# Kernel tuning notes

Hardware: AMD Instinct MI355X
Metric: run time of the kernel (lower is better)

The kernel has to match this reference:

```python
import jax, jax.numpy as jnp
import numpy as np

N_NODES = 50000
N_EDGES = 800000
D_IN, D_HID, D_OUT = 128, 96, 32


def _lin_params(key, d_in, d_out):
    k1, k2 = jax.random.split(key)
    bound = 1.0 / np.sqrt(d_in)
    W = jax.random.uniform(k1, (d_in, d_out), jnp.float32, -bound, bound)
    b = jax.random.uniform(k2, (d_out,), jnp.float32, -bound, bound)
    return W, b


def setup_inputs() -> dict:
    key = jax.random.key(0)
    ks = jax.random.split(key, 11)
    x = jax.random.normal(ks[0], (N_NODES, D_IN), jnp.float32)
    edge_index = jax.random.randint(ks[1], (2, N_EDGES), 0, N_NODES, jnp.int64)
    Wq1, bq1 = _lin_params(ks[2], D_IN, D_HID)
    Wk1, bk1 = _lin_params(ks[3], D_IN, D_HID)
    Wv1, bv1 = _lin_params(ks[4], D_IN, D_HID)
    Ws1, bs1 = _lin_params(ks[5], D_IN, D_HID)
    Wq2, bq2 = _lin_params(ks[6], D_HID, D_HID)
    Wk2, bk2 = _lin_params(ks[7], D_HID, D_HID)
    Wv2, bv2 = _lin_params(ks[8], D_HID, D_HID)
    Ws2, bs2 = _lin_params(ks[9], D_HID, D_HID)
    Wd, bd = _lin_params(ks[10], D_HID, D_OUT)
    return dict(x=x, edge_index=edge_index,
                Wq1=Wq1, bq1=bq1, Wk1=Wk1, bk1=bk1, Wv1=Wv1, bv1=bv1, Ws1=Ws1, bs1=bs1,
                Wq2=Wq2, bq2=bq2, Wk2=Wk2, bk2=bk2, Wv2=Wv2, bv2=bv2, Ws2=Ws2, bs2=bs2,
                Wd=Wd, bd=bd)


def transformer_conv(x, src, dst, Wq, bq, Wk, bk, Wv, bv, Ws, bs):
    # PyG TransformerConv, heads=1, concat=True, root_weight=True, edge_dim=None
    q = x @ Wq + bq  # [N, d]
    k = x @ Wk + bk
    v = x @ Wv + bv
    d = q.shape[-1]
    scale = 1.0 / np.sqrt(d).astype(np.float32)
    alpha = jnp.sum(q[dst] * k[src], axis=-1) * scale  # [E]
    # segment softmax over destination nodes
    m = jax.ops.segment_max(alpha, dst, num_segments=N_NODES)  # [N]
    e = jnp.exp(alpha - m[dst])
    s = jax.ops.segment_sum(e, dst, num_segments=N_NODES)
    w = e / (s[dst] + 1e-16)
    out = jax.ops.segment_sum(w[:, None] * v[src], dst, num_segments=N_NODES)  # [N, d]
    return out + x @ Ws + bs  # root/skip connection


def reference(x, edge_index,
              Wq1, bq1, Wk1, bk1, Wv1, bv1, Ws1, bs1,
              Wq2, bq2, Wk2, bk2, Wv2, bv2, Ws2, bs2,
              Wd, bd):
    src, dst = edge_index[0], edge_index[1]
    h = transformer_conv(x, src, dst, Wq1, bq1, Wk1, bk1, Wv1, bv1, Ws1, bs1)
    h = jax.nn.relu(h)
    h = transformer_conv(h, src, dst, Wq2, bq2, Wk2, bk2, Wv2, bv2, Ws2, bs2)
    return h @ Wd + bd
```

## Files before the change

kernel.cpp:

```cpp
#include <hip/hip_runtime.h>
#include <hip/hip_bf16.h>
#include <math.h>

#define NN_C 50000
#define NE_C 800000
#define NBKT 196
#define E_PER_BLK 4096
#define S1_BLOCKS 196
#define S2_CAP 8192

typedef short bf16x8 __attribute__((ext_vector_type(8)));
typedef float f32x4 __attribute__((ext_vector_type(4)));

__device__ inline float blo(unsigned int u) { return __uint_as_float(u << 16); }
__device__ inline float bhi(unsigned int u) { return __uint_as_float(u & 0xffff0000u); }

__device__ inline unsigned short bf16rne(float f) {
    union { __hip_bfloat16 h; unsigned short u; } c;
    c.h = __float2bfloat16(f);
    return c.u;
}
__device__ inline unsigned int pk2(float a, float b) {
    return (unsigned int)bf16rne(a) | ((unsigned int)bf16rne(b) << 16);
}

__device__ inline int block_incl_scan(int v, int lane, int wid, int* ws)
{
    int x = v;
    #pragma unroll
    for (int off = 1; off < 64; off <<= 1) {
        int t = __shfl_up(x, off);
        if (lane >= off) x += t;
    }
    if (lane == 63) ws[wid] = x;
    __syncthreads();
    int woff = 0;
    #pragma unroll
    for (int w = 0; w < 4; ++w)
        if (w < wid) woff += ws[w];
    return woff + x;
}

template<bool AF32>
__global__ __launch_bounds__(256) void gemm_mfma(
    const void* __restrict__ Ap, const unsigned short* __restrict__ Wt,
    const float* __restrict__ bias,
    unsigned short* __restrict__ aggb, unsigned short* __restrict__ qsb,
    int M)
{
    __shared__ char lds[65536];
    char* sA = lds;
    char* sB = lds + 32768;
    const int tid = threadIdx.x;
    const int r0 = blockIdx.x * 128;
    const int c0 = blockIdx.y * 128;
    const char* Wb = (const char*)Wt + (size_t)c0 * 256;

    if (AF32) {
        const char* Asrc = (const char*)Ap;
        #pragma unroll
        for (int sct = 0; sct < 8; ++sct) {
            int o = (sct * 256 + tid) * 16;
            int r = o >> 8;
            int gr = r0 + r; if (gr > M - 1) gr = M - 1;
            const char* p = Asrc + (size_t)gr * 512 + (o & 255) * 2;
            float4 a = *reinterpret_cast<const float4*>(p);
            float4 b = *reinterpret_cast<const float4*>(p + 16);
            uint4 val;
            val.x = pk2(a.x, a.y); val.y = pk2(a.z, a.w);
            val.z = pk2(b.x, b.y); val.w = pk2(b.z, b.w);
            *reinterpret_cast<uint4*>(sA + (o ^ ((r & 7) << 4))) = val;
        }
    } else {
        const char* Asrc = (const char*)Ap;
        #pragma unroll
        for (int sct = 0; sct < 8; ++sct) {
            int o = (sct * 256 + tid) * 16;
            int r = o >> 8;
            int gr = r0 + r; if (gr > M - 1) gr = M - 1;
            uint4 val = *reinterpret_cast<const uint4*>(Asrc + (size_t)gr * 256 + (o & 255));
            *reinterpret_cast<uint4*>(sA + (o ^ ((r & 7) << 4))) = val;
        }
    }
    #pragma unroll
    for (int sct = 0; sct < 8; ++sct) {
        int o = (sct * 256 + tid) * 16;
        int r = o >> 8;
        uint4 val = *reinterpret_cast<const uint4*>(Wb + o);
        *reinterpret_cast<uint4*>(sB + (o ^ ((r & 7) << 4))) = val;
    }
    __syncthreads();

    const int lane = tid & 63, wid = tid >> 6;
    const int wm = wid >> 1, wn = wid & 1;
    const int qw = lane >> 4, c16 = lane & 15;

    f32x4 acc[4][4];
    #pragma unroll
    for (int a = 0; a < 4; ++a)
        #pragma unroll
        for (int b = 0; b < 4; ++b) acc[a][b] = (f32x4){0.f, 0.f, 0.f, 0.f};

    int aoff[4], boff[4];
    #pragma unroll
    for (int fm = 0; fm < 4; ++fm) {
        int r = wm * 64 + fm * 16 + c16;
        aoff[fm] = r * 256 + ((qw * 16) ^ ((r & 7) << 4));
    }
    #pragma unroll
    for (int fn = 0; fn < 4; ++fn) {
        int r = wn * 64 + fn * 16 + c16;
        boff[fn] = r * 256 + ((qw * 16) ^ ((r & 7) << 4));
    }

    #pragma unroll
    for (int ks = 0; ks < 4; ++ks) {
        const int kx = ks * 64;
        bf16x8 af[4], bfr[4];
        #pragma unroll
        for (int fm = 0; fm < 4; ++fm)
            af[fm] = *reinterpret_cast<const bf16x8*>(sA + (aoff[fm] ^ kx));
        #pragma unroll
        for (int fn = 0; fn < 4; ++fn)
            bfr[fn] = *reinterpret_cast<const bf16x8*>(sB + (boff[fn] ^ kx));
        #pragma unroll
        for (int fm = 0; fm < 4; ++fm)
            #pragma unroll
            for (int fn = 0; fn < 4; ++fn)
                acc[fm][fn] = __builtin_amdgcn_mfma_f32_16x16x32_bf16(
                    af[fm], bfr[fn], acc[fm][fn], 0, 0, 0);
    }

    #pragma unroll
    for (int fn = 0; fn < 4; ++fn) {
        int colbase = c0 + wn * 64 + fn * 16;
        int g = colbase / 96;
        unsigned short* obuf; int elem0;
        if (g == 0)      { obuf = qsb;  elem0 = colbase; }
        else if (g == 3) { obuf = qsb;  elem0 = colbase - 192; }
        else             { obuf = aggb; elem0 = colbase - 96; }
        float bcol = bias[colbase + c16];
        #pragma unroll
        for (int fm = 0; fm < 4; ++fm) {
            #pragma unroll
            for (int j = 0; j < 4; ++j) {
                int rg = r0 + wm * 64 + fm * 16 + qw * 4 + j;
                float o = acc[fm][fn][j] + bcol;
                float o2 = __shfl_xor(o, 1);
                if (!(lane & 1) && rg < M) {
                    *reinterpret_cast<unsigned int*>(
                        (char*)obuf + (size_t)rg * 384 + (size_t)(elem0 + c16) * 2) = pk2(o, o2);
                }
            }
        }
    }
}

__global__ __launch_bounds__(256) void setup_kernel(
    const float* __restrict__ w0a, const float* __restrict__ w1a,
    const float* __restrict__ w2a, const float* __restrict__ w3a,
    const float* __restrict__ b0a, const float* __restrict__ b1a,
    const float* __restrict__ b2a, const float* __restrict__ b3a,
    const float* __restrict__ w0b, const float* __restrict__ w1b,
    const float* __restrict__ w2b, const float* __restrict__ w3b,
    const float* __restrict__ b0b, const float* __restrict__ b1b,
    const float* __restrict__ b2b, const float* __restrict__ b3b,
    const int* __restrict__ dst,
    unsigned short* __restrict__ WtA, float* __restrict__ b4a,
    unsigned short* __restrict__ WtB, float* __restrict__ b4b,
    int* __restrict__ bucketCnt)
{
    __shared__ int hist[NBKT];
    const int tid = threadIdx.x;
    const int blk = blockIdx.x;
    if (blk < 384) {
        const bool L2w = blk >= 192;
        int idx = (L2w ? blk - 192 : blk) * 256 + tid;
        int n = idx >> 7, k = idx & 127;
        int g = n / 96, c = n - g * 96;
        const float* w; const float* bb;
        if (!L2w) {
            w = (g == 0) ? w0a : (g == 1) ? w1a : (g == 2) ? w2a : w3a;
            bb = (g == 0) ? b0a : (g == 1) ? b1a : (g == 2) ? b2a : b3a;
            WtA[idx] = bf16rne((k < 128) ? w[(size_t)k * 96 + c] : 0.f);
            if (k == 0) b4a[n] = bb[c];
        } else {
            w = (g == 0) ? w0b : (g == 1) ? w1b : (g == 2) ? w2b : w3b;
            bb = (g == 0) ? b0b : (g == 1) ? b1b : (g == 2) ? b2b : b3b;
            WtB[idx] = bf16rne((k < 96) ? w[(size_t)k * 96 + c] : 0.f);
            if (k == 0) b4b[n] = bb[c];
        }
    } else {
        const int hb = blk - 384;
        for (int t = tid; t < NBKT; t += 256) hist[t] = 0;
        __syncthreads();
        const int e0 = hb * E_PER_BLK;
        const int ne = min(E_PER_BLK, NE_C - e0);
        for (int j = tid; j < ne; j += 256)
            atomicAdd(&hist[((unsigned)dst[e0 + j]) >> 8], 1);
        __syncthreads();
        for (int t = tid; t < NBKT; t += 256)
            if (hist[t]) atomicAdd(&bucketCnt[t], hist[t]);
    }
}

__global__ __launch_bounds__(256) void scanb_kernel(
    const int* __restrict__ bucketCnt, int* __restrict__ bucketBase,
    int* __restrict__ gCur)
{
    __shared__ int ws[4];
    const int tid = threadIdx.x;
    int v = (tid < NBKT) ? bucketCnt[tid] : 0;
    int incl = block_incl_scan(v, tid & 63, tid >> 6, ws);
    int excl = incl - v;
    if (tid < NBKT) { bucketBase[tid] = excl; gCur[tid] = excl; }
    if (tid == NBKT - 1) bucketBase[NBKT] = incl;
}

__global__ __launch_bounds__(256) void stage1_kernel(
    const int* __restrict__ src, const int* __restrict__ dst,
    int* __restrict__ gCur, unsigned int* __restrict__ bktArr)
{
    __shared__ int hist[NBKT], loff[NBKT], lcur[NBKT], gbase[NBKT];
    __shared__ unsigned int bufRaw[E_PER_BLK];
    __shared__ unsigned int buf[E_PER_BLK];
    __shared__ int ws[4];
    const int tid = threadIdx.x;
    const int e0 = blockIdx.x * E_PER_BLK;
    const int ne = min(E_PER_BLK, NE_C - e0);

    for (int t = tid; t < NBKT; t += 256) hist[t] = 0;
    __syncthreads();
    for (int j = tid; j < ne; j += 256) {
        int d = dst[e0 + j], s = src[e0 + j];
        unsigned int pk = ((unsigned)d << 16) | (unsigned)s;
        bufRaw[j] = pk;
        atomicAdd(&hist[(unsigned)d >> 8], 1);
    }
    __syncthreads();
    {
        int v = (tid < NBKT) ? hist[tid] : 0;
        int incl = block_incl_scan(v, tid & 63, tid >> 6, ws);
        if (tid < NBKT) { loff[tid] = incl - v; lcur[tid] = incl - v; }
    }
    __syncthreads();
    for (int j = tid; j < ne; j += 256) {
        unsigned int pk = bufRaw[j];
        int p = atomicAdd(&lcur[pk >> 24], 1);
        buf[p] = pk;
    }
    __syncthreads();
    if (tid < NBKT && hist[tid] > 0) gbase[tid] = atomicAdd(&gCur[tid], hist[tid]);
    __syncthreads();
    for (int j = tid; j < ne; j += 256) {
        unsigned int pk = buf[j];
        int b = pk >> 24;
        bktArr[gbase[b] + (j - loff[b])] = pk;
    }
}

__global__ __launch_bounds__(256) void stage2_kernel(
    const unsigned int* __restrict__ bktArr, const int* __restrict__ bucketBase,
    int* __restrict__ csr, int* __restrict__ row)
{
    __shared__ int ncnt[256], noff[256], ncur[256];
    __shared__ int outb[S2_CAP];
    __shared__ int ws[4];
    const int tid = threadIdx.x;
    const int b = blockIdx.x;
    const int base = bucketBase[b];
    const int cnt = bucketBase[b + 1] - base;

    ncnt[tid] = 0;
    __syncthreads();
    for (int j = tid; j < cnt; j += 256)
        atomicAdd(&ncnt[(bktArr[base + j] >> 16) & 255], 1);
    __syncthreads();
    {
        int v = ncnt[tid];
        int incl = block_incl_scan(v, tid & 63, tid >> 6, ws);
        noff[tid] = incl - v; ncur[tid] = incl - v;
    }
    __syncthreads();
    for (int j = tid; j < cnt; j += 256) {
        unsigned int pk = bktArr[base + j];
        int p = atomicAdd(&ncur[(pk >> 16) & 255], 1);
        if (p < S2_CAP) outb[p] = (int)(pk & 0xFFFFu);
    }
    __syncthreads();
    for (int j = tid; j < cnt && j < S2_CAP; j += 256) csr[base + j] = outb[j];
    const int node0 = b * 256;
    if (node0 + tid < NN_C) row[node0 + tid] = base + noff[tid];
    if (b == 0 && tid == 0) row[NN_C] = NE_C;
}

template<int MODE>
__global__ __launch_bounds__(256) void aggregate_kernel(
    const unsigned short* __restrict__ aggb, const unsigned short* __restrict__ qsb,
    const int* __restrict__ row, const int* __restrict__ csr,
    const float* __restrict__ Wd, const float* __restrict__ bd,
    void* __restrict__ outv, int nnodes)
{
    __shared__ float headL[MODE == 1 ? (96 * 32 + 32 + 4 * 96) : 1];
    const int tid  = threadIdx.x;
    const int wid  = tid >> 6;
    const int lane = tid & 63;
    const int c = lane & 31;
    const int h = lane >> 5;
    const int n = blockIdx.x * 4 + wid;

    if constexpr (MODE == 1) {
        for (int t = tid; t < 3072; t += 256) headL[t] = Wd[t];
        if (tid < 32) headL[3072 + tid] = bd[tid];
    }

    const float scale = 0.10206207261596577f;
    const char* AG = (const char*)aggb;
    const char* QS = (const char*)qsb;
    const size_t qrb = (size_t)n * 384;

    const unsigned int qa  = *(const unsigned int*)(QS + qrb + 4 * c);
    const unsigned int qbu = *(const unsigned int*)(QS + qrb + 128 + 4 * (c & 15));
    const float qalo = blo(qa), qahi = bhi(qa);
    float qblo, qbhi;
    if (c < 16) { qblo = blo(qbu); qbhi = bhi(qbu); } else { qblo = 0.f; qbhi = 0.f; }
    const int xsel = (c < 16) ? 128 : 256;

    float s = 0.f, alo = 0.f, ahi = 0.f, xlo = 0.f, xhi = 0.f;
    const int beg = row[n], end = row[n + 1];

    auto do_pair = [&](int i0) {
        const int s0 = csr[i0 + h], s1 = csr[i0 + 2 + h];
        const size_t b0 = (size_t)s0 * 384, b1 = (size_t)s1 * 384;
        unsigned int ka0 = *(const unsigned int*)(AG + b0 + 4 * c);
        unsigned int xb0 = *(const unsigned int*)(AG + b0 + xsel + 4 * c);
        unsigned int va0 = *(const unsigned int*)(AG + b0 + 192 + 4 * c);
        unsigned int ka1 = *(const unsigned int*)(AG + b1 + 4 * c);
        unsigned int xb1 = *(const unsigned int*)(AG + b1 + xsel + 4 * c);
        unsigned int va1 = *(const unsigned int*)(AG + b1 + 192 + 4 * c);
        float p0 = qalo * blo(ka0) + qahi * bhi(ka0) + qblo * blo(xb0) + qbhi * bhi(xb0);
        float p1 = qalo * blo(ka1) + qahi * bhi(ka1) + qblo * blo(xb1) + qbhi * bhi(xb1);
        #pragma unroll
        for (int off = 1; off < 32; off <<= 1) {
            p0 += __shfl_xor(p0, off);
            p1 += __shfl_xor(p1, off);
        }
        float e0 = __expf(p0 * scale);
        float e1 = __expf(p1 * scale);
        float eb0 = (c >= 16) ? e0 : 0.f;
        float eb1 = (c >= 16) ? e1 : 0.f;
        s   += e0 + e1;
        alo += e0 * blo(va0) + e1 * blo(va1);
        ahi += e0 * bhi(va0) + e1 * bhi(va1);
        xlo += eb0 * blo(xb0) + eb1 * blo(xb1);
        xhi += eb0 * bhi(xb0) + eb1 * bhi(xb1);
    };

    int i = beg;
    for (; i + 8 <= end; i += 8) { do_pair(i); do_pair(i + 4); }
    for (; i + 4 <= end; i += 4) do_pair(i);
    for (; i < end; i += 2) {
        const int j = i + h;
        const int jc = (j < end) ? j : (end - 1);
        const int sc = csr[jc];
        const size_t b = (size_t)sc * 384;
        unsigned int ka = *(const unsigned int*)(AG + b + 4 * c);
        unsigned int xb = *(const unsigned int*)(AG + b + xsel + 4 * c);
        unsigned int va = *(const unsigned int*)(AG + b + 192 + 4 * c);
        float p = qalo * blo(ka) + qahi * bhi(ka) + qblo * blo(xb) + qbhi * bhi(xb);
        #pragma unroll
        for (int off = 1; off < 32; off <<= 1) p += __shfl_xor(p, off);
        float e = (j < end) ? __expf(p * scale) : 0.f;
        float eb = (c >= 16) ? e : 0.f;
        s += e;
        alo += e * blo(va); ahi += e * bhi(va);
        xlo += eb * blo(xb); xhi += eb * bhi(xb);
    }
    s   += __shfl_xor(s, 32);
    alo += __shfl_xor(alo, 32);
    ahi += __shfl_xor(ahi, 32);
    xlo += __shfl_xor(xlo, 32);
    xhi += __shfl_xor(xhi, 32);
    const float inv = 1.0f / (s + 1e-16f);

    if constexpr (MODE == 0) {
        if (lane < 32) {
            const unsigned int sa = *(const unsigned int*)(QS + qrb + 192 + 4 * c);
            float o0 = fmaxf(alo * inv + blo(sa), 0.f);
            float o1 = fmaxf(ahi * inv + bhi(sa), 0.f);
            char* O = (char*)outv;
            const size_t ob = (size_t)n * 256;
            *(unsigned int*)(O + ob + 4 * c) = pk2(o0, o1);
            if (c >= 16) {
                const unsigned int sx = *(const unsigned int*)(QS + qrb + 256 + 4 * c);
                float ox0 = fmaxf(xlo * inv + blo(sx), 0.f);
                float ox1 = fmaxf(xhi * inv + bhi(sx), 0.f);
                *(unsigned int*)(O + ob + 64 + 4 * c) = pk2(ox0, ox1);
            } else {
                *(unsigned int*)(O + ob + 192 + 4 * c) = 0u;
            }
        }
    } else {
        float* oW = headL + 3104 + wid * 96;
        if (lane < 32) {
            const unsigned int sa = *(const unsigned int*)(QS + qrb + 192 + 4 * c);
            oW[2 * c]     = alo * inv + blo(sa);
            oW[2 * c + 1] = ahi * inv + bhi(sa);
            if (c >= 16) {
                const unsigned int sx = *(const unsigned int*)(QS + qrb + 256 + 4 * c);
                oW[2 * c + 32] = xlo * inv + blo(sx);
                oW[2 * c + 33] = xhi * inv + bhi(sx);
            }
        }
        __syncthreads();
        float acc = 0.f;
        const int d0 = h * 48;
        #pragma unroll
        for (int d = 0; d < 48; ++d)
            acc += oW[d0 + d] * headL[(d0 + d) * 32 + c];
        acc += __shfl_xor(acc, 32);
        if (lane < 32)
            ((float*)outv)[(size_t)n * 32 + c] = acc + headL[3072 + c];
    }
}

extern "C" void kernel_launch(void* const* d_in, const int* in_sizes, int n_in,
                              void* d_out, int out_size, void* d_ws, size_t ws_size,
                              hipStream_t stream)
{
    const int NN = NN_C, NE = NE_C;
    const float* x  = (const float*)d_in[0];
    const int*   ei = (const int*)d_in[1];
    const int* src = ei;
    const int* dst = ei + NE;

    const float* Wq1 = (const float*)d_in[2];  const float* bq1 = (const float*)d_in[3];
    const float* Wk1 = (const float*)d_in[4];  const float* bk1 = (const float*)d_in[5];
    const float* Wv1 = (const float*)d_in[6];  const float* bv1 = (const float*)d_in[7];
    const float* Ws1 = (const float*)d_in[8];  const float* bs1 = (const float*)d_in[9];
    const float* Wq2 = (const float*)d_in[10]; const float* bq2 = (const float*)d_in[11];
    const float* Wk2 = (const float*)d_in[12]; const float* bk2 = (const float*)d_in[13];
    const float* Wv2 = (const float*)d_in[14]; const float* bv2 = (const float*)d_in[15];
    const float* Ws2 = (const float*)d_in[16]; const float* bs2 = (const float*)d_in[17];
    const float* Wd  = (const float*)d_in[18]; const float* bd  = (const float*)d_in[19];

    char* base = (char*)d_ws;
    size_t off = 0;
    auto alloc = [&](size_t bytes) -> void* {
        void* p = base + off;
        off += (bytes + 255) & ~(size_t)255;
        return p;
    };
    unsigned short* aggb   = (unsigned short*)alloc((size_t)NN * 192 * 2);
    unsigned short* qsb    = (unsigned short*)alloc((size_t)NN * 192 * 2);
    unsigned short* hb16   = (unsigned short*)alloc((size_t)NN * 128 * 2);
    unsigned short* Wt4a   = (unsigned short*)alloc(384 * 128 * 2);
    unsigned short* Wt4b   = (unsigned short*)alloc(384 * 128 * 2);
    float*          b4a    = (float*)alloc(384 * 4);
    float*          b4b    = (float*)alloc(384 * 4);
    int*            bucketCnt  = (int*)alloc(NBKT * 4);
    int*            bucketBase = (int*)alloc((NBKT + 1) * 4);
    int*            gCur   = (int*)alloc(NBKT * 4);
    unsigned int*   bktArr = (unsigned int*)alloc((size_t)NE * 4);
    int*            csr    = (int*)alloc((size_t)NE * 4);
    int*            rowp   = (int*)alloc((NN + 1) * 4);

    hipMemsetAsync(bucketCnt, 0, NBKT * sizeof(int), stream);
    setup_kernel<<<384 + S1_BLOCKS, 256, 0, stream>>>(
        Wq1, Wk1, Wv1, Ws1, bq1, bk1, bv1, bs1,
        Wq2, Wk2, Wv2, Ws2, bq2, bk2, bv2, bs2,
        dst, Wt4a, b4a, Wt4b, b4b, bucketCnt);
    scanb_kernel<<<1, 256, 0, stream>>>(bucketCnt, bucketBase, gCur);
    stage1_kernel<<<S1_BLOCKS, 256, 0, stream>>>(src, dst, gCur, bktArr);
    stage2_kernel<<<NBKT, 256, 0, stream>>>(bktArr, bucketBase, csr, rowp);

    dim3 blk(256);
    dim3 gg((NN + 127) / 128, 3);
    const int aggGrid = NN / 4;

    gemm_mfma<true><<<gg, blk, 0, stream>>>(x, Wt4a, b4a, aggb, qsb, NN);
    aggregate_kernel<0><<<aggGrid, blk, 0, stream>>>(
        aggb, qsb, rowp, csr, nullptr, nullptr, hb16, NN);

    gemm_mfma<false><<<gg, blk, 0, stream>>>(hb16, Wt4b, b4b, aggb, qsb, NN);
    aggregate_kernel<1><<<aggGrid, blk, 0, stream>>>(
        aggb, qsb, rowp, csr, Wd, bd, d_out, NN);
}
```

Before: 304.1 us.

## Process four edges per wave with 16 lanes each and precomputed byte offsets

The aggregation kernel now splits each 64-lane wave into four groups of 16 lanes, each handling one edge. Each lane loads 12 bytes of the key and value rows, replacing the earlier 32-lanes-per-edge scheme with its split k/v tail handling. The CSR array now stores src*384 byte offsets so no multiply is needed per edge, and the attention scale is folded into q. This aims to raise memory-level parallelism and cut shuffle and ALU work per edge. The cost is wider final cross-group reductions and unaligned 12-byte loads.

```diff
diff --git a/kernel.cpp b/kernel.cpp
--- a/kernel.cpp
+++ b/kernel.cpp
@@ -11,6 +11,8 @@
 
 typedef short bf16x8 __attribute__((ext_vector_type(8)));
 typedef float f32x4 __attribute__((ext_vector_type(4)));
+
+struct U3 { unsigned int x, y, z; };
 
 __device__ inline float blo(unsigned int u) { return __uint_as_float(u << 16); }
 __device__ inline float bhi(unsigned int u) { return __uint_as_float(u & 0xffff0000u); }
@@ -261,7 +263,7 @@
 
 __global__ __launch_bounds__(256) void stage2_kernel(
     const unsigned int* __restrict__ bktArr, const int* __restrict__ bucketBase,
-    int* __restrict__ csr, int* __restrict__ row)
+    int* __restrict__ csrb, int* __restrict__ row)
 {
     __shared__ int ncnt[256], noff[256], ncur[256];
     __shared__ int outb[S2_CAP];
@@ -285,10 +287,10 @@
     for (int j = tid; j < cnt; j += 256) {
         unsigned int pk = bktArr[base + j];
         int p = atomicAdd(&ncur[(pk >> 16) & 255], 1);
-        if (p < S2_CAP) outb[p] = (int)(pk & 0xFFFFu);
-    }
-    __syncthreads();
-    for (int j = tid; j < cnt && j < S2_CAP; j += 256) csr[base + j] = outb[j];
+        if (p < S2_CAP) outb[p] = (int)(pk & 0xFFFFu) * 384;
+    }
+    __syncthreads();
+    for (int j = tid; j < cnt && j < S2_CAP; j += 256) csrb[base + j] = outb[j];
     const int node0 = b * 256;
     if (node0 + tid < NN_C) row[node0 + tid] = base + noff[tid];
     if (b == 0 && tid == 0) row[NN_C] = NE_C;
@@ -297,7 +299,7 @@
 template<int MODE>
 __global__ __launch_bounds__(256) void aggregate_kernel(
     const unsigned short* __restrict__ aggb, const unsigned short* __restrict__ qsb,
-    const int* __restrict__ row, const int* __restrict__ csr,
+    const int* __restrict__ row, const int* __restrict__ csrb,
     const float* __restrict__ Wd, const float* __restrict__ bd,
     void* __restrict__ outv, int nnodes)
 {
@@ -305,13 +307,15 @@
     const int tid  = threadIdx.x;
     const int wid  = tid >> 6;
     const int lane = tid & 63;
-    const int c = lane & 31;
-    const int h = lane >> 5;
+    const int l = lane & 15;
+    const int q = lane >> 4;
     const int n = blockIdx.x * 4 + wid;
 
     if constexpr (MODE == 1) {
-        for (int t = tid; t < 3072; t += 256) headL[t] = Wd[t];
+        #pragma unroll
+        for (int t = 0; t < 12; ++t) headL[t * 256 + tid] = Wd[t * 256 + tid];
         if (tid < 32) headL[3072 + tid] = bd[tid];
+        __syncthreads();
     }
 
     const float scale = 0.10206207261596577f;
@@ -319,102 +323,86 @@
     const char* QS = (const char*)qsb;
     const size_t qrb = (size_t)n * 384;
 
-    const unsigned int qa  = *(const unsigned int*)(QS + qrb + 4 * c);
-    const unsigned int qbu = *(const unsigned int*)(QS + qrb + 128 + 4 * (c & 15));
-    const float qalo = blo(qa), qahi = bhi(qa);
-    float qblo, qbhi;
-    if (c < 16) { qblo = blo(qbu); qbhi = bhi(qbu); } else { qblo = 0.f; qbhi = 0.f; }
-    const int xsel = (c < 16) ? 128 : 256;
-
-    float s = 0.f, alo = 0.f, ahi = 0.f, xlo = 0.f, xhi = 0.f;
+    U3 qd = *(const U3*)(QS + qrb + 12 * l);
+    const float q0 = blo(qd.x) * scale, q1 = bhi(qd.x) * scale;
+    const float q2 = blo(qd.y) * scale, q3 = bhi(qd.y) * scale;
+    const float q4 = blo(qd.z) * scale, q5 = bhi(qd.z) * scale;
+
+    const char* AGk = AG + 12 * l;
+    const char* AGv = AG + 192 + 12 * l;
+
+    float s = 0.f, a0 = 0.f, a1 = 0.f, a2 = 0.f, a3 = 0.f, a4 = 0.f, a5 = 0.f;
     const int beg = row[n], end = row[n + 1];
 
-    auto do_pair = [&](int i0) {
-        const int s0 = csr[i0 + h], s1 = csr[i0 + 2 + h];
-        const size_t b0 = (size_t)s0 * 384, b1 = (size_t)s1 * 384;
-        unsigned int ka0 = *(const unsigned int*)(AG + b0 + 4 * c);
-        unsigned int xb0 = *(const unsigned int*)(AG + b0 + xsel + 4 * c);
-        unsigned int va0 = *(const unsigned int*)(AG + b0 + 192 + 4 * c);
-        unsigned int ka1 = *(const unsigned int*)(AG + b1 + 4 * c);
-        unsigned int xb1 = *(const unsigned int*)(AG + b1 + xsel + 4 * c);
-        unsigned int va1 = *(const unsigned int*)(AG + b1 + 192 + 4 * c);
-        float p0 = qalo * blo(ka0) + qahi * bhi(ka0) + qblo * blo(xb0) + qbhi * bhi(xb0);
-        float p1 = qalo * blo(ka1) + qahi * bhi(ka1) + qblo * blo(xb1) + qbhi * bhi(xb1);
-        #pragma unroll
-        for (int off = 1; off < 32; off <<= 1) {
-            p0 += __shfl_xor(p0, off);
-            p1 += __shfl_xor(p1, off);
-        }
-        float e0 = __expf(p0 * scale);
-        float e1 = __expf(p1 * scale);
-        float eb0 = (c >= 16) ? e0 : 0.f;
-        float eb1 = (c >= 16) ? e1 : 0.f;
-        s   += e0 + e1;
-        alo += e0 * blo(va0) + e1 * blo(va1);
-        ahi += e0 * bhi(va0) + e1 * bhi(va1);
-        xlo += eb0 * blo(xb0) + eb1 * blo(xb1);
-        xhi += eb0 * bhi(xb0) + eb1 * bhi(xb1);
+    auto quad = [&](int i0) {
+        const int base = csrb[i0 + q];
+        U3 kd = *(const U3*)(AGk + base);
+        U3 vd = *(const U3*)(AGv + base);
+        float p = q0 * blo(kd.x) + q1 * bhi(kd.x) + q2 * blo(kd.y)
+                + q3 * bhi(kd.y) + q4 * blo(kd.z) + q5 * bhi(kd.z);
+        #pragma unroll
+        for (int off = 1; off < 16; off <<= 1) p += __shfl_xor(p, off);
+        float e = __expf(p);
+        s  += e;
+        a0 += e * blo(vd.x); a1 += e * bhi(vd.x);
+        a2 += e * blo(vd.y); a3 += e * bhi(vd.y);
+        a4 += e * blo(vd.z); a5 += e * bhi(vd.z);
     };
 
     int i = beg;
-    for (; i + 8 <= end; i += 8) { do_pair(i); do_pair(i + 4); }
-    for (; i + 4 <= end; i += 4) do_pair(i);
-    for (; i < end; i += 2) {
-        const int j = i + h;
+    for (; i + 8 <= end; i += 8) { quad(i); quad(i + 4); }
+    for (; i + 4 <= end; i += 4) quad(i);
+    if (i < end) {
+        const int j = i + q;
         const int jc = (j < end) ? j : (end - 1);
-        const int sc = csr[jc];
-        const size_t b = (size_t)sc * 384;
-        unsigned int ka = *(const unsigned int*)(AG + b + 4 * c);
-        unsigned int xb = *(const unsigned int*)(AG + b + xsel + 4 * c);
-        unsigned int va = *(const unsigned int*)(AG + b + 192 + 4 * c);
-        float p = qalo * blo(ka) + qahi * bhi(ka) + qblo * blo(xb) + qbhi * bhi(xb);
-        #pragma unroll
-        for (int off = 1; off < 32; off <<= 1) p += __shfl_xor(p, off);
-        float e = (j < end) ? __expf(p * scale) : 0.f;
-        float eb = (c >= 16) ? e : 0.f;
-        s += e;
-        alo += e * blo(va); ahi += e * bhi(va);
-        xlo += eb * blo(xb); xhi += eb * bhi(xb);
-    }
-    s   += __shfl_xor(s, 32);
-    alo += __shfl_xor(alo, 32);
-    ahi += __shfl_xor(ahi, 32);
-    xlo += __shfl_xor(xlo, 32);
-    xhi += __shfl_xor(xhi, 32);
+        const int base = csrb[jc];
+        U3 kd = *(const U3*)(AGk + base);
+        U3 vd = *(const U3*)(AGv + base);
+        float p = q0 * blo(kd.x) + q1 * bhi(kd.x) + q2 * blo(kd.y)
+                + q3 * bhi(kd.y) + q4 * blo(kd.z) + q5 * bhi(kd.z);
+        #pragma unroll
+        for (int off = 1; off < 16; off <<= 1) p += __shfl_xor(p, off);
+        float e = (j < end) ? __expf(p) : 0.f;
+        s  += e;
+        a0 += e * blo(vd.x); a1 += e * bhi(vd.x);
+        a2 += e * blo(vd.y); a3 += e * bhi(vd.y);
+        a4 += e * blo(vd.z); a5 += e * bhi(vd.z);
+    }
+    #pragma unroll
+    for (int off = 16; off < 64; off <<= 1) {
+        s  += __shfl_xor(s, off);
+        a0 += __shfl_xor(a0, off); a1 += __shfl_xor(a1, off);
+        a2 += __shfl_xor(a2, off); a3 += __shfl_xor(a3, off);
+        a4 += __shfl_xor(a4, off); a5 += __shfl_xor(a5, off);
+    }
     const float inv = 1.0f / (s + 1e-16f);
 
+    U3 sd = *(const U3*)(QS + qrb + 192 + 12 * l);
+    float o0 = a0 * inv + blo(sd.x), o1 = a1 * inv + bhi(sd.x);
+    float o2 = a2 * inv + blo(sd.y), o3 = a3 * inv + bhi(sd.y);
+    float o4 = a4 * inv + blo(sd.z), o5 = a5 * inv + bhi(sd.z);
+
     if constexpr (MODE == 0) {
-        if (lane < 32) {
-            const unsigned int sa = *(const unsigned int*)(QS + qrb + 192 + 4 * c);
-            float o0 = fmaxf(alo * inv + blo(sa), 0.f);
-            float o1 = fmaxf(ahi * inv + bhi(sa), 0.f);
-            char* O = (char*)outv;
-            const size_t ob = (size_t)n * 256;
-            *(unsigned int*)(O + ob + 4 * c) = pk2(o0, o1);
-            if (c >= 16) {
-                const unsigned int sx = *(const unsigned int*)(QS + qrb + 256 + 4 * c);
-                float ox0 = fmaxf(xlo * inv + blo(sx), 0.f);
-                float ox1 = fmaxf(xhi * inv + bhi(sx), 0.f);
-                *(unsigned int*)(O + ob + 64 + 4 * c) = pk2(ox0, ox1);
-            } else {
-                *(unsigned int*)(O + ob + 192 + 4 * c) = 0u;
-            }
+        o0 = fmaxf(o0, 0.f); o1 = fmaxf(o1, 0.f); o2 = fmaxf(o2, 0.f);
+        o3 = fmaxf(o3, 0.f); o4 = fmaxf(o4, 0.f); o5 = fmaxf(o5, 0.f);
+        char* O = (char*)outv;
+        const size_t ob = (size_t)n * 256;
+        if (q < 3) {
+            float u0 = (q == 0) ? o0 : (q == 1) ? o2 : o4;
+            float u1 = (q == 0) ? o1 : (q == 1) ? o3 : o5;
+            *(unsigned int*)(O + ob + 12 * l + 4 * q) = pk2(u0, u1);
+        } else {
+            *(unsigned int*)(O + ob + 192 + 4 * l) = 0u;
         }
     } else {
         float* oW = headL + 3104 + wid * 96;
-        if (lane < 32) {
-            const unsigned int sa = *(const unsigned int*)(QS + qrb + 192 + 4 * c);
-            oW[2 * c]     = alo * inv + blo(sa);
-            oW[2 * c + 1] = ahi * inv + bhi(sa);
-            if (c >= 16) {
-                const unsigned int sx = *(const unsigned int*)(QS + qrb + 256 + 4 * c);
-                oW[2 * c + 32] = xlo * inv + blo(sx);
-                oW[2 * c + 33] = xhi * inv + bhi(sx);
-            }
-        }
-        __syncthreads();
+        if (q == 0) {
+            oW[6 * l + 0] = o0; oW[6 * l + 1] = o1; oW[6 * l + 2] = o2;
+            oW[6 * l + 3] = o3; oW[6 * l + 4] = o4; oW[6 * l + 5] = o5;
+        }
+        const int c = lane & 31, h = lane >> 5;
+        const int d0 = h * 48;
         float acc = 0.f;
-        const int d0 = h * 48;
         #pragma unroll
         for (int d = 0; d < 48; ++d)
             acc += oW[d0 + d] * headL[(d0 + d) * 32 + c];
@@ -462,7 +450,7 @@
     int*            bucketBase = (int*)alloc((NBKT + 1) * 4);
     int*            gCur   = (int*)alloc(NBKT * 4);
     unsigned int*   bktArr = (unsigned int*)alloc((size_t)NE * 4);
-    int*            csr    = (int*)alloc((size_t)NE * 4);
+    int*            csrb   = (int*)alloc((size_t)NE * 4);
     int*            rowp   = (int*)alloc((NN + 1) * 4);
 
     hipMemsetAsync(bucketCnt, 0, NBKT * sizeof(int), stream);
@@ -472,7 +460,7 @@
         dst, Wt4a, b4a, Wt4b, b4b, bucketCnt);
     scanb_kernel<<<1, 256, 0, stream>>>(bucketCnt, bucketBase, gCur);
     stage1_kernel<<<S1_BLOCKS, 256, 0, stream>>>(src, dst, gCur, bktArr);
-    stage2_kernel<<<NBKT, 256, 0, stream>>>(bktArr, bucketBase, csr, rowp);
+    stage2_kernel<<<NBKT, 256, 0, stream>>>(bktArr, bucketBase, csrb, rowp);
 
     dim3 blk(256);
     dim3 gg((NN + 127) / 128, 3);
@@ -480,9 +468,9 @@
 
     gemm_mfma<true><<<gg, blk, 0, stream>>>(x, Wt4a, b4a, aggb, qsb, NN);
     aggregate_kernel<0><<<aggGrid, blk, 0, stream>>>(
-        aggb, qsb, rowp, csr, nullptr, nullptr, hb16, NN);
+        aggb, qsb, rowp, csrb, nullptr, nullptr, hb16, NN);
 
     gemm_mfma<false><<<gg, blk, 0, stream>>>(hb16, Wt4b, b4b, aggb, qsb, NN);
     aggregate_kernel<1><<<aggGrid, blk, 0, stream>>>(
-        aggb, qsb, rowp, csr, Wd, bd, d_out, NN);
-}
+        aggb, qsb, rowp, csrb, Wd, bd, d_out, NN);
+}
```

New measurement: 285.3 us. -6.2%, faster.
